# Performance work log

Measured on AMD Instinct MI355X. Metric: run time of the kernel, lower is better.

Reference implementation:

```python
import jax, jax.numpy as jnp
import numpy as np

B, L, S, D, H, TOPK = 8, 2048, 1000, 1024, 8, 10
E = D // H  # d_keys = 128


def setup_inputs() -> dict:
    key = jax.random.key(0)
    ks = jax.random.split(key, 8)
    s = 1.0 / np.sqrt(D)
    return {
        "target_embedding": jax.random.normal(ks[0], (B, L, D), dtype=jnp.float32),
        "source_embedding": jax.random.normal(ks[1], (S, D), dtype=jnp.float32),
        "Wq": jax.random.normal(ks[2], (D, D), dtype=jnp.float32) * s,
        "bq": jnp.zeros((D,), dtype=jnp.float32),
        "Wk": jax.random.normal(ks[3], (D, D), dtype=jnp.float32) * s,
        "bk": jnp.zeros((D,), dtype=jnp.float32),
        "Wo": jax.random.normal(ks[4], (D, D), dtype=jnp.float32) * s,
        "bo": jnp.zeros((D,), dtype=jnp.float32),
        "data_id": 0,
    }


def reference(target_embedding, source_embedding, Wq, bq, Wk, bk, Wo, bo, data_id):
    # data_id is unused by the original module's math.
    b, l, d = target_embedding.shape
    h, e, topk = H, E, TOPK
    scale = 1.0 / np.sqrt(e)

    q = (target_embedding @ Wq + bq).reshape(b, l, h, e)   # [B,L,H,E]
    k = (source_embedding @ Wk + bk).reshape(-1, h, e)      # [S,H,E]

    scores = jnp.einsum('blhe,she->bhls', q, k)             # [B,H,L,S]
    A = jax.nn.softmax(scale * scores, axis=-1)             # dropout is eval-mode identity
    tmps = A.sum(axis=2)                                    # [B,H,S] head-wise column mass
    _, idxs = jax.lax.top_k(tmps, topk)                     # [B,H,topk]

    kh = jnp.transpose(k, (1, 0, 2))                        # [H,S,E]
    # gather per (batch, head) the topk source key vectors
    tok = kh[jnp.arange(h)[None, :, None], idxs, :]         # [B,H,topk,E]
    tok = jnp.transpose(tok, (0, 2, 1, 3)).reshape(b, topk, h * e)  # [B,topk,D]
    return tok @ Wo + bo                                    # [B,topk,D]
```

## Files before the change

kernel.cpp:

```cpp
#include <hip/hip_runtime.h>
#include <hip/hip_bf16.h>
#include <math.h>

constexpr int B_ = 8;
constexpr int L_ = 2048;
constexpr int S_ = 1000;
constexpr int D_ = 1024;
constexpr int H_ = 8;
constexpr int E_ = 128;
constexpr int TOPK_ = 10;
constexpr float SCALE_LOG2E_ = 0.12751744f;

typedef __attribute__((ext_vector_type(8))) short short8;
typedef __attribute__((ext_vector_type(4))) float f32x4;

__device__ inline unsigned short f2bf(float x) {
    unsigned u = __float_as_uint(x);
    unsigned r = (u + 0x7fffu + ((u >> 16) & 1u)) >> 16;
    return (unsigned short)r;
}
__device__ inline float bf2f(unsigned short s) {
    return __uint_as_float(((unsigned)s) << 16);
}

__device__ __forceinline__ float fexp2(float x) {
#if __has_builtin(__builtin_amdgcn_exp2f)
    return __builtin_amdgcn_exp2f(x);
#else
    return __expf(x * 0.69314718056f);
#endif
}

typedef __attribute__((address_space(1))) const unsigned int gas_u32;
typedef __attribute__((address_space(3))) unsigned int las_u32;
__device__ __forceinline__ void gload_lds16(const void* g, void* l) {
    __builtin_amdgcn_global_load_lds((gas_u32*)g, (las_u32*)l, 16, 0, 0);
}

__global__ __launch_bounds__(256) void gemm_bias_kernel(
    const float* __restrict__ A, const float* __restrict__ Bm,
    const float* __restrict__ bias, float* __restrict__ C,
    int M, int N, int Kd)
{
    __shared__ float As[16][65];
    __shared__ float Bs[16][68];

    const int t  = threadIdx.x;
    const int tx = t & 15;
    const int ty = t >> 4;
    const int m0 = blockIdx.y * 64;
    const int n0 = blockIdx.x * 64;

    float acc[4][4];
#pragma unroll
    for (int i = 0; i < 4; ++i)
#pragma unroll
        for (int j = 0; j < 4; ++j) acc[i][j] = 0.f;

    for (int k0 = 0; k0 < Kd; k0 += 16) {
        {
            const int row = t >> 2;
            const int c4  = (t & 3) * 4;
            float4 v = {0.f, 0.f, 0.f, 0.f};
            if (m0 + row < M)
                v = *(const float4*)&A[(size_t)(m0 + row) * Kd + k0 + c4];
            As[c4 + 0][row] = v.x;
            As[c4 + 1][row] = v.y;
            As[c4 + 2][row] = v.z;
            As[c4 + 3][row] = v.w;
        }
        {
            const int row = t >> 4;
            const int c4  = (t & 15) * 4;
            float4 v = *(const float4*)&Bm[(size_t)(k0 + row) * N + n0 + c4];
            *(float4*)&Bs[row][c4] = v;
        }
        __syncthreads();
#pragma unroll
        for (int k = 0; k < 16; ++k) {
            float a[4], b[4];
#pragma unroll
            for (int i = 0; i < 4; ++i) a[i] = As[k][ty * 4 + i];
            float4 bv = *(const float4*)&Bs[k][tx * 4];
            b[0] = bv.x; b[1] = bv.y; b[2] = bv.z; b[3] = bv.w;
#pragma unroll
            for (int i = 0; i < 4; ++i)
#pragma unroll
                for (int j = 0; j < 4; ++j) acc[i][j] += a[i] * b[j];
        }
        __syncthreads();
    }

#pragma unroll
    for (int i = 0; i < 4; ++i) {
        const int row = m0 + ty * 4 + i;
        if (row < M) {
#pragma unroll
            for (int j = 0; j < 4; ++j) {
                const int col = n0 + tx * 4 + j;
                C[(size_t)row * N + col] = acc[i][j] + bias[col];
            }
        }
    }
}

__global__ __launch_bounds__(256) void splitWT_kernel(
    const float* __restrict__ W,
    unsigned short* __restrict__ WTh, unsigned short* __restrict__ WTl)
{
    __shared__ __attribute__((aligned(16))) float tile[64][68];
    const int t  = threadIdx.x;
    const int k0 = blockIdx.y * 64, n0 = blockIdx.x * 64;
#pragma unroll
    for (int it = 0; it < 4; ++it) {
        int id = it * 256 + t;
        int r = id >> 4, c = id & 15;
        *(float4*)&tile[r][c * 4] = *(const float4*)&W[(size_t)(k0 + r) * D_ + n0 + c * 4];
    }
    __syncthreads();
#pragma unroll
    for (int it = 0; it < 4; ++it) {
        int id = it * 256 + t;
        int n = id >> 4, c = id & 15;
        unsigned short hs[4], ls[4];
#pragma unroll
        for (int i = 0; i < 4; ++i) {
            float x = tile[c * 4 + i][n];
            hs[i] = f2bf(x);
            ls[i] = f2bf(x - bf2f(hs[i]));
        }
        size_t o = (size_t)(n0 + n) * D_ + k0 + c * 4;
        uint2 uh; uh.x = (unsigned)hs[0] | ((unsigned)hs[1] << 16);
                  uh.y = (unsigned)hs[2] | ((unsigned)hs[3] << 16);
        uint2 ul; ul.x = (unsigned)ls[0] | ((unsigned)ls[1] << 16);
                  ul.y = (unsigned)ls[2] | ((unsigned)ls[3] << 16);
        *(uint2*)&WTh[o] = uh;
        *(uint2*)&WTl[o] = ul;
    }
}

__global__ __launch_bounds__(256) void split_src_kernel(
    const float* __restrict__ src,
    unsigned short* __restrict__ Sh, unsigned short* __restrict__ Sl)
{
    int idx  = blockIdx.x * 256 + threadIdx.x;
    int base = idx * 4;
    int row  = base >> 10;
    float4 v = {0.f, 0.f, 0.f, 0.f};
    if (row < S_) v = *(const float4*)&src[base];
    float xs[4] = {v.x, v.y, v.z, v.w};
    unsigned short hs[4], ls[4];
#pragma unroll
    for (int i = 0; i < 4; ++i) {
        hs[i] = f2bf(xs[i]);
        ls[i] = f2bf(xs[i] - bf2f(hs[i]));
    }
    uint2 uh; uh.x = (unsigned)hs[0] | ((unsigned)hs[1] << 16);
              uh.y = (unsigned)hs[2] | ((unsigned)hs[3] << 16);
    uint2 ul; ul.x = (unsigned)ls[0] | ((unsigned)ls[1] << 16);
              ul.y = (unsigned)ls[2] | ((unsigned)ls[3] << 16);
    *(uint2*)&Sh[base] = uh;
    *(uint2*)&Sl[base] = ul;
}

__global__ __launch_bounds__(256, 2) void kproj_kernel(
    const unsigned short* __restrict__ Sh, const unsigned short* __restrict__ Sl,
    const unsigned short* __restrict__ WkTh, const unsigned short* __restrict__ WkTl,
    const float* __restrict__ bk,
    float* __restrict__ Kbuf,
    unsigned short* __restrict__ Kh, unsigned short* __restrict__ Kl)
{
    __shared__ __attribute__((aligned(16))) unsigned short Ah[128 * 64];
    __shared__ __attribute__((aligned(16))) unsigned short Al[128 * 64];
    __shared__ __attribute__((aligned(16))) unsigned short Bh[128 * 64];
    __shared__ __attribute__((aligned(16))) unsigned short Bl[128 * 64];

    const int t    = threadIdx.x;
    const int lane = t & 63, w = t >> 6;
    const int mb   = blockIdx.x >> 3;
    const int n0   = (blockIdx.x & 7) * 128;

    f32x4 acc[2][8];
#pragma unroll
    for (int m = 0; m < 2; ++m)
#pragma unroll
        for (int n = 0; n < 8; ++n) acc[m][n] = (f32x4){0.f, 0.f, 0.f, 0.f};

    for (int k0 = 0; k0 < D_; k0 += 64) {
        __syncthreads();
#pragma unroll
        for (int it = 0; it < 4; ++it) {
            int r = it * 32 + (t >> 3), c = t & 7;
            size_t gofs = (size_t)r * D_ + k0 + ((c ^ (r & 7)) << 3);
            int db = it * 4096 + t * 16;
            gload_lds16(&Sh[(size_t)(mb * 128) * D_ + gofs], (char*)Ah + db);
            gload_lds16(&Sl[(size_t)(mb * 128) * D_ + gofs], (char*)Al + db);
            gload_lds16(&WkTh[(size_t)n0 * D_ + gofs], (char*)Bh + db);
            gload_lds16(&WkTl[(size_t)n0 * D_ + gofs], (char*)Bl + db);
        }
        __syncthreads();

#pragma unroll
        for (int ki = 0; ki < 2; ++ki) {
            short8 ah[2], al[2];
#pragma unroll
            for (int m = 0; m < 2; ++m) {
                int r = w * 32 + m * 16 + (lane & 15);
                int slot = ki * 4 + (lane >> 4);
                int lofs = r * 64 + ((slot ^ (r & 7)) << 3);
                ah[m] = *(short8*)&Ah[lofs];
                al[m] = *(short8*)&Al[lofs];
            }
#pragma unroll
            for (int n = 0; n < 8; ++n) {
                int nn = n * 16 + (lane & 15);
                int slot = ki * 4 + (lane >> 4);
                int lofs = nn * 64 + ((slot ^ (nn & 7)) << 3);
                short8 bh = *(short8*)&Bh[lofs];
                short8 bl = *(short8*)&Bl[lofs];
#pragma unroll
                for (int m = 0; m < 2; ++m) {
                    acc[m][n] = __builtin_amdgcn_mfma_f32_16x16x32_bf16(ah[m], bh, acc[m][n], 0, 0, 0);
                    acc[m][n] = __builtin_amdgcn_mfma_f32_16x16x32_bf16(ah[m], bl, acc[m][n], 0, 0, 0);
                    acc[m][n] = __builtin_amdgcn_mfma_f32_16x16x32_bf16(al[m], bh, acc[m][n], 0, 0, 0);
                }
            }
        }
    }

#pragma unroll
    for (int n = 0; n < 8; ++n) {
        int col = n0 + n * 16 + (lane & 15);
        float bkv = bk[col];
#pragma unroll
        for (int m = 0; m < 2; ++m) {
            int rbase = mb * 128 + w * 32 + m * 16 + ((lane >> 4) << 2);
#pragma unroll
            for (int r = 0; r < 4; ++r) {
                int row = rbase + r;
                unsigned short hh = 0, ll = 0;
                if (row < S_) {
                    float kv = acc[m][n][r] + bkv;
                    Kbuf[(size_t)row * D_ + col] = kv;
                    hh = f2bf(kv);
                    ll = f2bf(kv - bf2f(hh));
                }
                Kh[(size_t)row * D_ + col] = hh;
                Kl[(size_t)row * D_ + col] = ll;
            }
        }
    }
}

__global__ __launch_bounds__(256, 2) void qproj_kernel(
    const float* __restrict__ tgt,
    const unsigned short* __restrict__ WqTh, const unsigned short* __restrict__ WqTl,
    const float* __restrict__ bq,
    unsigned short* __restrict__ qhb, unsigned short* __restrict__ qlb)
{
    __shared__ __attribute__((aligned(16))) float          Af[2][128 * 32];
    __shared__ __attribute__((aligned(16))) unsigned short Bh[2][128 * 32];
    __shared__ __attribute__((aligned(16))) unsigned short Bl[2][128 * 32];

    const int t    = threadIdx.x;
    const int lane = t & 63, w = t >> 6;
    const int x    = blockIdx.x & 7;
    const int jj   = blockIdx.x >> 3;
    const int n0   = (jj & 7) * 128;
    const int mb   = (jj >> 3) * 8 + x;

    f32x4 acc[2][8];
#pragma unroll
    for (int m = 0; m < 2; ++m)
#pragma unroll
        for (int n = 0; n < 8; ++n) acc[m][n] = (f32x4){0.f, 0.f, 0.f, 0.f};

#define QP_ISSUE(KT, BUF)                                                   \
    do {                                                                    \
        _Pragma("unroll")                                                   \
        for (int it = 0; it < 4; ++it) {                       \
            int id = it * 256 + t;                                          \
            int line = id >> 4, sub = id & 15;                              \
            int gs = sub ^ (line & 15);                                     \
            size_t ga = (size_t)(mb * 128 + line * 2 + (gs >> 3)) * D_      \
                        + (KT) * 32 + ((gs & 7) << 2);                      \
            gload_lds16(&tgt[ga], (char*)&Af[(BUF)][0] + id * 16);          \
        }                                                                   \
        _Pragma("unroll")                                                   \
        for (int it = 0; it < 2; ++it) {                      \
            int id = it * 256 + t;                                          \
            int line = id >> 4, sub = id & 15;                              \
            int gs = sub ^ (line & 15);                                     \
            size_t gb = (size_t)(n0 + line * 4 + (gs >> 2)) * D_            \
                        + (KT) * 32 + ((gs & 3) << 3);                      \
            gload_lds16(&WqTh[gb], (char*)&Bh[(BUF)][0] + id * 16);         \
            gload_lds16(&WqTl[gb], (char*)&Bl[(BUF)][0] + id * 16);         \
        }                                                                   \
    } while (0)

    QP_ISSUE(0, 0);
    int cur = 0;
    for (int kt = 0; kt < 32; ++kt) {
        __syncthreads();
        if (kt < 31) QP_ISSUE(kt + 1, cur ^ 1);

        short8 ah[2], al[2];
#pragma unroll
        for (int m = 0; m < 2; ++m) {
            int r    = w * 32 + m * 16 + (lane & 15);
            int c0   = (lane >> 4) * 2;
            int line = r >> 1;
            int sub0 = (r & 1) * 8 + c0;
            float4 x0 = *(float4*)&Af[cur][line * 64 + ((sub0 ^ (line & 15)) << 2)];
            float4 x1 = *(float4*)&Af[cur][line * 64 + (((sub0 + 1) ^ (line & 15)) << 2)];
            float xs[8] = {x0.x, x0.y, x0.z, x0.w, x1.x, x1.y, x1.z, x1.w};
#pragma unroll
            for (int jjj = 0; jjj < 8; ++jjj) {
                unsigned short hh = f2bf(xs[jjj]);
                ah[m][jjj] = (short)hh;
                al[m][jjj] = (short)f2bf(xs[jjj] - bf2f(hh));
            }
        }
#pragma unroll
        for (int n = 0; n < 8; ++n) {
            int nn   = n * 16 + (lane & 15);
            int line = nn >> 2;
            int sub  = (nn & 3) * 4 + (lane >> 4);
            int lofs = line * 128 + ((sub ^ (line & 15)) << 3);
            short8 bh = *(short8*)&Bh[cur][lofs];
            short8 bl = *(short8*)&Bl[cur][lofs];
#pragma unroll
            for (int m = 0; m < 2; ++m) {
                acc[m][n] = __builtin_amdgcn_mfma_f32_16x16x32_bf16(ah[m], bh, acc[m][n], 0, 0, 0);
                acc[m][n] = __builtin_amdgcn_mfma_f32_16x16x32_bf16(ah[m], bl, acc[m][n], 0, 0, 0);
                acc[m][n] = __builtin_amdgcn_mfma_f32_16x16x32_bf16(al[m], bh, acc[m][n], 0, 0, 0);
            }
        }
        cur ^= 1;
    }
#undef QP_ISSUE

#pragma unroll
    for (int n = 0; n < 8; ++n) {
        int col = n0 + n * 16 + (lane & 15);
        float bqv = bq[col];
#pragma unroll
        for (int m = 0; m < 2; ++m) {
            int rbase = mb * 128 + w * 32 + m * 16 + ((lane >> 4) << 2);
#pragma unroll
            for (int r = 0; r < 4; ++r) {
                float q = (acc[m][n][r] + bqv) * SCALE_LOG2E_;
                unsigned short hh = f2bf(q);
                qhb[(size_t)(rbase + r) * D_ + col] = hh;
                qlb[(size_t)(rbase + r) * D_ + col] = f2bf(q - bf2f(hh));
            }
        }
    }
}

__global__ __launch_bounds__(256, 2) void scores2p_kernel(
    const unsigned short* __restrict__ qhb, const unsigned short* __restrict__ qlb,
    const unsigned short* __restrict__ Kh, const unsigned short* __restrict__ Kl,
    float* __restrict__ tmps, int b0)
{
    __shared__ __attribute__((aligned(16))) unsigned short SH[2][32 * 128];
    __shared__ __attribute__((aligned(16))) unsigned short SL[2][32 * 128];
    __shared__ float tmps_l[1024];

    const int t    = threadIdx.x;
    const int lane = t & 63, w = t >> 6;
    const int blk  = blockIdx.x;
    const int bb   = blk >> 6;
    const int h    = (blk >> 3) & 7;
    const int lt   = blk & 7;
    const int qrow0 = bb * L_ + lt * 256;
    const int bh_i  = (b0 + bb) * H_ + h;
    const int kr0   = t >> 4;
    const int kc0   = t & 15;

    for (int i = t; i < 1024; i += 256) tmps_l[i] = 0.f;

#define SC_ISSUE0(ST, BUF)                                                  \
    do {                                                                    \
        _Pragma("unroll")                                                   \
        for (int it = 0; it < 4; ++it) {                                    \
            int r = it * 16 + kr0;                                          \
            size_t g = (size_t)((ST) * 64 + r) * D_ + h * E_                \
                       + ((kc0 ^ (r & 15)) << 3);                           \
            char* base = (it < 2) ? (char*)&SH[(BUF)][0]                    \
                                  : (char*)&SL[(BUF)][0];                   \
            int db = (it & 1) * 4096 + t * 16;                              \
            gload_lds16(&Kh[g], base + db);                                 \
        }                                                                   \
    } while (0)

#define SC_ISSUE2(ST, BUF)                                                  \
    do {                                                                    \
        _Pragma("unroll")                                                   \
        for (int it = 0; it < 2; ++it) {                                    \
            int r = it * 16 + kr0;                                          \
            size_t g = (size_t)((ST) * 32 + r) * D_ + h * E_                \
                       + ((kc0 ^ (r & 15)) << 3);                           \
            int db = it * 4096 + t * 16;                                    \
            gload_lds16(&Kh[g], (char*)&SH[(BUF)][0] + db);                 \
            gload_lds16(&Kl[g], (char*)&SL[(BUF)][0] + db);                 \
        }                                                                   \
    } while (0)

    SC_ISSUE0(0, 1);

    short8 qh[4][4], ql[4][4];
#pragma unroll
    for (int ch = 0; ch < 8; ++ch) {
        __syncthreads();
#pragma unroll
        for (int it = 0; it < 2; ++it) {
            int r = it * 16 + kr0;
            size_t g = (size_t)(qrow0 + ch * 32 + r) * D_ + h * E_ + kc0 * 8;
            int lofs = r * 128 + ((kc0 ^ (r & 15)) << 3);
            *(uint4*)&SH[0][lofs] = *(const uint4*)&qhb[g];
            *(uint4*)&SL[0][lofs] = *(const uint4*)&qlb[g];
        }
        __syncthreads();
        if ((ch >> 1) == w) {
#pragma unroll
            for (int j = 0; j < 2; ++j) {
                int rg = (ch & 1) * 2 + j;
#pragma unroll
                for (int ki = 0; ki < 4; ++ki) {
                    int rq = j * 16 + (lane & 15);
                    int slot = ki * 4 + (lane >> 4);
                    int lofs = rq * 128 + ((slot ^ (rq & 15)) << 3);
                    qh[rg][ki] = *(short8*)&SH[0][lofs];
                    ql[rg][ki] = *(short8*)&SL[0][lofs];
                }
            }
        }
    }

    float zacc[4][4];
#pragma unroll
    for (int rg = 0; rg < 4; ++rg)
#pragma unroll
        for (int r = 0; r < 4; ++r) zacc[rg][r] = 0.f;
    float invZ[4][4];

    int cur = 1;

    for (int u = 0; u < 16; ++u) {
        __syncthreads();
        if (u < 15) SC_ISSUE0(u + 1, cur ^ 1);
        else        SC_ISSUE2(0, cur ^ 1);

#pragma unroll
        for (int nfh = 0; nfh < 2; ++nfh) {
            f32x4 acc[4][2];
#pragma unroll
            for (int rg = 0; rg < 4; ++rg)
#pragma unroll
                for (int n2 = 0; n2 < 2; ++n2) acc[rg][n2] = (f32x4){0.f, 0.f, 0.f, 0.f};

#pragma unroll
            for (int ki = 0; ki < 4; ++ki)
#pragma unroll
                for (int n2 = 0; n2 < 2; ++n2) {
                    int nf = nfh * 2 + n2;
                    int sr = nf * 16 + (lane & 15);
                    int slot = ki * 4 + (lane >> 4);
                    int lofs = (sr & 31) * 128 + ((slot ^ (sr & 15)) << 3);
                    short8 bh = (nf < 2) ? *(short8*)&SH[cur][lofs]
                                         : *(short8*)&SL[cur][lofs];
#pragma unroll
                    for (int rg = 0; rg < 4; ++rg)
                        acc[rg][n2] = __builtin_amdgcn_mfma_f32_16x16x32_bf16(qh[rg][ki], bh, acc[rg][n2], 0, 0, 0);
                }

#pragma unroll
            for (int n2 = 0; n2 < 2; ++n2) {
                int s = u * 64 + (nfh * 2 + n2) * 16 + (lane & 15);
                if (s < S_) {
#pragma unroll
                    for (int rg = 0; rg < 4; ++rg)
#pragma unroll
                        for (int r = 0; r < 4; ++r)
                            zacc[rg][r] += fexp2(acc[rg][n2][r]);
                }
            }
        }

        if (u == 15) {
#pragma unroll
            for (int rg = 0; rg < 4; ++rg)
#pragma unroll
                for (int r = 0; r < 4; ++r) {
                    float z = zacc[rg][r];
                    z += __shfl_xor(z, 1);
                    z += __shfl_xor(z, 2);
                    z += __shfl_xor(z, 4);
                    z += __shfl_xor(z, 8);
                    invZ[rg][r] = 1.f / z;
                }
        }
        cur ^= 1;
    }

    for (int u = 0; u < 32; ++u) {
        __syncthreads();
        if (u < 31) SC_ISSUE2(u + 1, cur ^ 1);

        f32x4 acc[4][2];
#pragma unroll
        for (int rg = 0; rg < 4; ++rg)
#pragma unroll
            for (int nf = 0; nf < 2; ++nf) acc[rg][nf] = (f32x4){0.f, 0.f, 0.f, 0.f};

#pragma unroll
        for (int ki = 0; ki < 4; ++ki)
#pragma unroll
            for (int nf = 0; nf < 2; ++nf) {
                int sr = nf * 16 + (lane & 15);
                int slot = ki * 4 + (lane >> 4);
                int lofs = sr * 128 + ((slot ^ (sr & 15)) << 3);
                short8 bh = *(short8*)&SH[cur][lofs];
                short8 bl = *(short8*)&SL[cur][lofs];
#pragma unroll
                for (int rg = 0; rg < 4; ++rg) {
                    acc[rg][nf] = __builtin_amdgcn_mfma_f32_16x16x32_bf16(qh[rg][ki], bh, acc[rg][nf], 0, 0, 0);
                    acc[rg][nf] = __builtin_amdgcn_mfma_f32_16x16x32_bf16(qh[rg][ki], bl, acc[rg][nf], 0, 0, 0);
                    acc[rg][nf] = __builtin_amdgcn_mfma_f32_16x16x32_bf16(ql[rg][ki], bh, acc[rg][nf], 0, 0, 0);
                }
            }

#pragma unroll
        for (int nf = 0; nf < 2; ++nf) {
            int s = u * 32 + nf * 16 + (lane & 15);
            if (s < S_) {
                float val = 0.f;
#pragma unroll
                for (int rg = 0; rg < 4; ++rg)
#pragma unroll
                    for (int r = 0; r < 4; ++r)
                        val += fexp2(acc[rg][nf][r]) * invZ[rg][r];
                atomicAdd(&tmps_l[s], val);
            }
        }
        cur ^= 1;
    }
#undef SC_ISSUE0
#undef SC_ISSUE2

    __syncthreads();
    for (int i = t; i < S_; i += 256)
        atomicAdd(&tmps[(size_t)bh_i * S_ + i], tmps_l[i]);
}

__global__ __launch_bounds__(256) void topk_kernel(
    const float* __restrict__ tmps, int* __restrict__ idxs)
{
    const int bh = blockIdx.x;
    const int t  = threadIdx.x;
    __shared__ float v[S_];
    __shared__ float rv[256];
    __shared__ int   ri[256];

    for (int i = t; i < S_; i += 256) v[i] = tmps[(size_t)bh * S_ + i];
    __syncthreads();

    for (int it = 0; it < TOPK_; ++it) {
        float best = -1e38f;
        int bi = 0x7fffffff;
        for (int s = t; s < S_; s += 256) {
            const float x = v[s];
            if (x > best) { best = x; bi = s; }
        }
        rv[t] = best; ri[t] = bi;
        __syncthreads();
        for (int k = 128; k > 0; k >>= 1) {
            if (t < k) {
                const float x = rv[t + k];
                const int  xi = ri[t + k];
                if (x > rv[t] || (x == rv[t] && xi < ri[t])) { rv[t] = x; ri[t] = xi; }
            }
            __syncthreads();
        }
        if (t == 0) {
            idxs[bh * TOPK_ + it] = ri[0];
            v[ri[0]] = -1e38f;
        }
        __syncthreads();
    }
}

__global__ __launch_bounds__(256) void gather_kernel(
    const float* __restrict__ K, const int* __restrict__ idxs,
    float* __restrict__ tok)
{
    const int o = blockIdx.x * 256 + threadIdx.x;
    if (o >= B_ * TOPK_ * D_) return;
    const int d  = o & (D_ - 1);
    const int tt = (o >> 10) % TOPK_;
    const int b  = o / (D_ * TOPK_);
    const int h  = d >> 7;
    const int s  = idxs[(b * H_ + h) * TOPK_ + tt];
    tok[o] = K[(size_t)s * D_ + d];
}

extern "C" void kernel_launch(void* const* d_in, const int* in_sizes, int n_in,
                              void* d_out, int out_size, void* d_ws, size_t ws_size,
                              hipStream_t stream)
{
    const float* tgt = (const float*)d_in[0];
    const float* src = (const float*)d_in[1];
    const float* Wq  = (const float*)d_in[2];
    const float* bq  = (const float*)d_in[3];
    const float* Wk  = (const float*)d_in[4];
    const float* bk  = (const float*)d_in[5];
    const float* Wo  = (const float*)d_in[6];
    const float* bo  = (const float*)d_in[7];
    float* out = (float*)d_out;

    char* ws = (char*)d_ws;
    size_t off = 0;
    float*          Kbuf = (float*)(ws + off);          off += (size_t)S_ * D_ * 4;
    float*          tmps = (float*)(ws + off);          off += (size_t)B_ * H_ * S_ * 4;
    int*            idxs = (int*)(ws + off);            off += (size_t)B_ * H_ * TOPK_ * 4;
    off = (off + 255) & ~(size_t)255;
    float*          tok  = (float*)(ws + off);          off += (size_t)B_ * TOPK_ * D_ * 4;
    unsigned short* Kh   = (unsigned short*)(ws + off); off += (size_t)1024 * D_ * 2;
    unsigned short* Kl   = (unsigned short*)(ws + off); off += (size_t)1024 * D_ * 2;
    unsigned short* WqTh = (unsigned short*)(ws + off); off += (size_t)D_ * D_ * 2;
    unsigned short* WqTl = (unsigned short*)(ws + off); off += (size_t)D_ * D_ * 2;
    unsigned short* WkTh = (unsigned short*)(ws + off); off += (size_t)D_ * D_ * 2;
    unsigned short* WkTl = (unsigned short*)(ws + off); off += (size_t)D_ * D_ * 2;
    unsigned short* Sh   = (unsigned short*)(ws + off); off += (size_t)1024 * D_ * 2;
    unsigned short* Sl   = (unsigned short*)(ws + off); off += (size_t)1024 * D_ * 2;
    unsigned short* planes = (unsigned short*)(ws + off);
    const size_t fixed_bytes = off;
    const size_t plane_elems_per_b = (size_t)L_ * D_;

    int nb_fit = 1;
    if (ws_size > fixed_bytes) {
        size_t f = (ws_size - fixed_bytes) / (2 * plane_elems_per_b * 2);
        nb_fit = (f < 1) ? 1 : (f > 8 ? 8 : (int)f);
    }

    hipMemsetAsync(tmps, 0, (size_t)B_ * H_ * S_ * sizeof(float), stream);

    split_src_kernel<<<(1024 * D_) / (256 * 4), 256, 0, stream>>>(src, Sh, Sl);
    {
        dim3 g(D_ / 64, D_ / 64);
        splitWT_kernel<<<g, 256, 0, stream>>>(Wq, WqTh, WqTl);
        splitWT_kernel<<<g, 256, 0, stream>>>(Wk, WkTh, WkTl);
    }

    kproj_kernel<<<64, 256, 0, stream>>>(Sh, Sl, WkTh, WkTl, bk, Kbuf, Kh, Kl);

    for (int b0 = 0; b0 < B_; b0 += nb_fit) {
        int nb = (B_ - b0 < nb_fit) ? (B_ - b0) : nb_fit;
        unsigned short* qhb = planes;
        unsigned short* qlb = qhb + (size_t)nb_fit * plane_elems_per_b;

        qproj_kernel<<<nb * 128, 256, 0, stream>>>(
            tgt + (size_t)b0 * L_ * D_, WqTh, WqTl, bq, qhb, qlb);
        scores2p_kernel<<<nb * 64, 256, 0, stream>>>(qhb, qlb, Kh, Kl, tmps, b0);
    }

    topk_kernel<<<B_ * H_, 256, 0, stream>>>(tmps, idxs);
    gather_kernel<<<(B_ * TOPK_ * D_ + 255) / 256, 256, 0, stream>>>(Kbuf, idxs, tok);
    {
        dim3 g(D_ / 64, (B_ * TOPK_ + 63) / 64);
        gemm_bias_kernel<<<g, 256, 0, stream>>>(tok, Wo, bo, out, B_ * TOPK_, D_, D_);
    }
}
```

Before: 381.9 us.

## Load Q-projection activations to registers and enlarge score-pass K tiles

The Q projection no longer stages fp32 activations through shared memory. It loads them straight from global memory into registers, double-buffered across an explicitly unrolled pair of k-steps, and raises the occupancy hint to 3 blocks per CU because LDS use drops. The scores kernel's second pass now processes 64 source rows per stage in a unified 4-plane LDS buffer instead of 32, halving the barrier and issue count. The trade-off is higher register pressure and uncoalesced per-lane global reads of the activations.

```diff
diff --git a/kernel.cpp b/kernel.cpp
--- a/kernel.cpp
+++ b/kernel.cpp
@@ -252,13 +252,12 @@
     }
 }
 
-__global__ __launch_bounds__(256, 2) void qproj_kernel(
+__global__ __launch_bounds__(256, 3) void qproj_kernel(
     const float* __restrict__ tgt,
     const unsigned short* __restrict__ WqTh, const unsigned short* __restrict__ WqTl,
     const float* __restrict__ bq,
     unsigned short* __restrict__ qhb, unsigned short* __restrict__ qlb)
 {
-    __shared__ __attribute__((aligned(16))) float          Af[2][128 * 32];
     __shared__ __attribute__((aligned(16))) unsigned short Bh[2][128 * 32];
     __shared__ __attribute__((aligned(16))) unsigned short Bl[2][128 * 32];
 
@@ -275,19 +274,10 @@
 #pragma unroll
         for (int n = 0; n < 8; ++n) acc[m][n] = (f32x4){0.f, 0.f, 0.f, 0.f};
 
-#define QP_ISSUE(KT, BUF)                                                   \
+#define QB_ISSUE(KT, BUF)                                                   \
     do {                                                                    \
         _Pragma("unroll")                                                   \
-        for (int it = 0; it < 4; ++it) {                       \
-            int id = it * 256 + t;                                          \
-            int line = id >> 4, sub = id & 15;                              \
-            int gs = sub ^ (line & 15);                                     \
-            size_t ga = (size_t)(mb * 128 + line * 2 + (gs >> 3)) * D_      \
-                        + (KT) * 32 + ((gs & 7) << 2);                      \
-            gload_lds16(&tgt[ga], (char*)&Af[(BUF)][0] + id * 16);          \
-        }                                                                   \
-        _Pragma("unroll")                                                   \
-        for (int it = 0; it < 2; ++it) {                      \
+        for (int it = 0; it < 2; ++it) {                                    \
             int id = it * 256 + t;                                          \
             int line = id >> 4, sub = id & 15;                              \
             int gs = sub ^ (line & 15);                                     \
@@ -298,47 +288,65 @@
         }                                                                   \
     } while (0)
 
-    QP_ISSUE(0, 0);
-    int cur = 0;
-    for (int kt = 0; kt < 32; ++kt) {
-        __syncthreads();
-        if (kt < 31) QP_ISSUE(kt + 1, cur ^ 1);
-
-        short8 ah[2], al[2];
-#pragma unroll
-        for (int m = 0; m < 2; ++m) {
-            int r    = w * 32 + m * 16 + (lane & 15);
-            int c0   = (lane >> 4) * 2;
-            int line = r >> 1;
-            int sub0 = (r & 1) * 8 + c0;
-            float4 x0 = *(float4*)&Af[cur][line * 64 + ((sub0 ^ (line & 15)) << 2)];
-            float4 x1 = *(float4*)&Af[cur][line * 64 + (((sub0 + 1) ^ (line & 15)) << 2)];
-            float xs[8] = {x0.x, x0.y, x0.z, x0.w, x1.x, x1.y, x1.z, x1.w};
-#pragma unroll
-            for (int jjj = 0; jjj < 8; ++jjj) {
-                unsigned short hh = f2bf(xs[jjj]);
-                ah[m][jjj] = (short)hh;
-                al[m][jjj] = (short)f2bf(xs[jjj] - bf2f(hh));
-            }
-        }
-#pragma unroll
-        for (int n = 0; n < 8; ++n) {
-            int nn   = n * 16 + (lane & 15);
-            int line = nn >> 2;
-            int sub  = (nn & 3) * 4 + (lane >> 4);
-            int lofs = line * 128 + ((sub ^ (line & 15)) << 3);
-            short8 bh = *(short8*)&Bh[cur][lofs];
-            short8 bl = *(short8*)&Bl[cur][lofs];
-#pragma unroll
-            for (int m = 0; m < 2; ++m) {
-                acc[m][n] = __builtin_amdgcn_mfma_f32_16x16x32_bf16(ah[m], bh, acc[m][n], 0, 0, 0);
-                acc[m][n] = __builtin_amdgcn_mfma_f32_16x16x32_bf16(ah[m], bl, acc[m][n], 0, 0, 0);
-                acc[m][n] = __builtin_amdgcn_mfma_f32_16x16x32_bf16(al[m], bh, acc[m][n], 0, 0, 0);
-            }
-        }
-        cur ^= 1;
-    }
-#undef QP_ISSUE
+#define QA_LOAD(KT, XA)                                                     \
+    do {                                                                    \
+        _Pragma("unroll")                                                   \
+        for (int m = 0; m < 2; ++m) {                                       \
+            int r = mb * 128 + w * 32 + m * 16 + (lane & 15);               \
+            const float* ga = &tgt[(size_t)r * D_ + (KT) * 32 + (lane >> 4) * 8]; \
+            XA[m][0] = *(const float4*)ga;                                  \
+            XA[m][1] = *(const float4*)(ga + 4);                            \
+        }                                                                   \
+    } while (0)
+
+#define QP_COMPUTE(XA, BUF)                                                 \
+    do {                                                                    \
+        short8 ah[2], al[2];                                                \
+        _Pragma("unroll")                                                   \
+        for (int m = 0; m < 2; ++m) {                                       \
+            float xs[8] = {XA[m][0].x, XA[m][0].y, XA[m][0].z, XA[m][0].w,  \
+                           XA[m][1].x, XA[m][1].y, XA[m][1].z, XA[m][1].w}; \
+            _Pragma("unroll")                                               \
+            for (int j = 0; j < 8; ++j) {                                   \
+                unsigned short hh = f2bf(xs[j]);                            \
+                ah[m][j] = (short)hh;                                       \
+                al[m][j] = (short)f2bf(xs[j] - bf2f(hh));                   \
+            }                                                               \
+        }                                                                   \
+        _Pragma("unroll")                                                   \
+        for (int n = 0; n < 8; ++n) {                                       \
+            int nn   = n * 16 + (lane & 15);                                \
+            int line = nn >> 2;                                             \
+            int sub  = (nn & 3) * 4 + (lane >> 4);                          \
+            int lofs = line * 128 + ((sub ^ (line & 15)) << 3);             \
+            short8 bh = *(short8*)&Bh[(BUF)][lofs];                         \
+            short8 bl = *(short8*)&Bl[(BUF)][lofs];                         \
+            _Pragma("unroll")                                               \
+            for (int m = 0; m < 2; ++m) {                                   \
+                acc[m][n] = __builtin_amdgcn_mfma_f32_16x16x32_bf16(ah[m], bh, acc[m][n], 0, 0, 0); \
+                acc[m][n] = __builtin_amdgcn_mfma_f32_16x16x32_bf16(ah[m], bl, acc[m][n], 0, 0, 0); \
+                acc[m][n] = __builtin_amdgcn_mfma_f32_16x16x32_bf16(al[m], bh, acc[m][n], 0, 0, 0); \
+            }                                                               \
+        }                                                                   \
+    } while (0)
+
+    float4 xa0[2][2], xa1[2][2];
+    QB_ISSUE(0, 0);
+    QA_LOAD(0, xa0);
+
+#pragma unroll 1
+    for (int kt2 = 0; kt2 < 16; ++kt2) {
+        const int kt = kt2 * 2;
+        __syncthreads();
+        if (kt + 1 < 32) { QB_ISSUE(kt + 1, 1); QA_LOAD(kt + 1, xa1); }
+        QP_COMPUTE(xa0, 0);
+        __syncthreads();
+        if (kt + 2 < 32) { QB_ISSUE(kt + 2, 0); QA_LOAD(kt + 2, xa0); }
+        QP_COMPUTE(xa1, 1);
+    }
+#undef QB_ISSUE
+#undef QA_LOAD
+#undef QP_COMPUTE
 
 #pragma unroll
     for (int n = 0; n < 8; ++n) {
@@ -363,8 +371,7 @@
     const unsigned short* __restrict__ Kh, const unsigned short* __restrict__ Kl,
     float* __restrict__ tmps, int b0)
 {
-    __shared__ __attribute__((aligned(16))) unsigned short SH[2][32 * 128];
-    __shared__ __attribute__((aligned(16))) unsigned short SL[2][32 * 128];
+    __shared__ __attribute__((aligned(16))) unsigned short KB[2][4][32 * 128];
     __shared__ float tmps_l[1024];
 
     const int t    = threadIdx.x;
@@ -387,23 +394,22 @@
             int r = it * 16 + kr0;                                          \
             size_t g = (size_t)((ST) * 64 + r) * D_ + h * E_                \
                        + ((kc0 ^ (r & 15)) << 3);                           \
-            char* base = (it < 2) ? (char*)&SH[(BUF)][0]                    \
-                                  : (char*)&SL[(BUF)][0];                   \
             int db = (it & 1) * 4096 + t * 16;                              \
-            gload_lds16(&Kh[g], base + db);                                 \
+            gload_lds16(&Kh[g], (char*)&KB[(BUF)][it >> 1][0] + db);        \
         }                                                                   \
     } while (0)
 
-#define SC_ISSUE2(ST, BUF)                                                  \
+#define SC_ISSUE1(ST, BUF)                                                  \
     do {                                                                    \
         _Pragma("unroll")                                                   \
-        for (int it = 0; it < 2; ++it) {                                    \
+        for (int it = 0; it < 4; ++it) {                                    \
             int r = it * 16 + kr0;                                          \
-            size_t g = (size_t)((ST) * 32 + r) * D_ + h * E_                \
+            size_t g = (size_t)((ST) * 64 + r) * D_ + h * E_                \
                        + ((kc0 ^ (r & 15)) << 3);                           \
-            int db = it * 4096 + t * 16;                                    \
-            gload_lds16(&Kh[g], (char*)&SH[(BUF)][0] + db);                 \
-            gload_lds16(&Kl[g], (char*)&SL[(BUF)][0] + db);                 \
+            int pl = it >> 1;                                               \
+            int db = (it & 1) * 4096 + t * 16;                              \
+            gload_lds16(&Kh[g], (char*)&KB[(BUF)][pl][0] + db);             \
+            gload_lds16(&Kl[g], (char*)&KB[(BUF)][pl + 2][0] + db);         \
         }                                                                   \
     } while (0)
 
@@ -418,8 +424,8 @@
             int r = it * 16 + kr0;
             size_t g = (size_t)(qrow0 + ch * 32 + r) * D_ + h * E_ + kc0 * 8;
             int lofs = r * 128 + ((kc0 ^ (r & 15)) << 3);
-            *(uint4*)&SH[0][lofs] = *(const uint4*)&qhb[g];
-            *(uint4*)&SL[0][lofs] = *(const uint4*)&qlb[g];
+            *(uint4*)&KB[0][0][lofs] = *(const uint4*)&qhb[g];
+            *(uint4*)&KB[0][1][lofs] = *(const uint4*)&qlb[g];
         }
         __syncthreads();
         if ((ch >> 1) == w) {
@@ -431,8 +437,8 @@
                     int rq = j * 16 + (lane & 15);
                     int slot = ki * 4 + (lane >> 4);
                     int lofs = rq * 128 + ((slot ^ (rq & 15)) << 3);
-                    qh[rg][ki] = *(short8*)&SH[0][lofs];
-                    ql[rg][ki] = *(short8*)&SL[0][lofs];
+                    qh[rg][ki] = *(short8*)&KB[0][0][lofs];
+                    ql[rg][ki] = *(short8*)&KB[0][1][lofs];
                 }
             }
         }
@@ -450,7 +456,7 @@
     for (int u = 0; u < 16; ++u) {
         __syncthreads();
         if (u < 15) SC_ISSUE0(u + 1, cur ^ 1);
-        else        SC_ISSUE2(0, cur ^ 1);
+        else        SC_ISSUE1(0, cur ^ 1);
 
 #pragma unroll
         for (int nfh = 0; nfh < 2; ++nfh) {
@@ -468,8 +474,7 @@
                     int sr = nf * 16 + (lane & 15);
                     int slot = ki * 4 + (lane >> 4);
                     int lofs = (sr & 31) * 128 + ((slot ^ (sr & 15)) << 3);
-                    short8 bh = (nf < 2) ? *(short8*)&SH[cur][lofs]
-                                         : *(short8*)&SL[cur][lofs];
+                    short8 bh = *(short8*)&KB[cur][sr >> 5][lofs];
 #pragma unroll
                     for (int rg = 0; rg < 4; ++rg)
                         acc[rg][n2] = __builtin_amdgcn_mfma_f32_16x16x32_bf16(qh[rg][ki], bh, acc[rg][n2], 0, 0, 0);
@@ -504,50 +509,55 @@
         cur ^= 1;
     }
 
-    for (int u = 0; u < 32; ++u) {
-        __syncthreads();
-        if (u < 31) SC_ISSUE2(u + 1, cur ^ 1);
-
-        f32x4 acc[4][2];
-#pragma unroll
-        for (int rg = 0; rg < 4; ++rg)
-#pragma unroll
-            for (int nf = 0; nf < 2; ++nf) acc[rg][nf] = (f32x4){0.f, 0.f, 0.f, 0.f};
-
-#pragma unroll
-        for (int ki = 0; ki < 4; ++ki)
-#pragma unroll
-            for (int nf = 0; nf < 2; ++nf) {
-                int sr = nf * 16 + (lane & 15);
-                int slot = ki * 4 + (lane >> 4);
-                int lofs = sr * 128 + ((slot ^ (sr & 15)) << 3);
-                short8 bh = *(short8*)&SH[cur][lofs];
-                short8 bl = *(short8*)&SL[cur][lofs];
-#pragma unroll
-                for (int rg = 0; rg < 4; ++rg) {
-                    acc[rg][nf] = __builtin_amdgcn_mfma_f32_16x16x32_bf16(qh[rg][ki], bh, acc[rg][nf], 0, 0, 0);
-                    acc[rg][nf] = __builtin_amdgcn_mfma_f32_16x16x32_bf16(qh[rg][ki], bl, acc[rg][nf], 0, 0, 0);
-                    acc[rg][nf] = __builtin_amdgcn_mfma_f32_16x16x32_bf16(ql[rg][ki], bh, acc[rg][nf], 0, 0, 0);
-                }
-            }
-
-#pragma unroll
-        for (int nf = 0; nf < 2; ++nf) {
-            int s = u * 32 + nf * 16 + (lane & 15);
-            if (s < S_) {
-                float val = 0.f;
-#pragma unroll
-                for (int rg = 0; rg < 4; ++rg)
-#pragma unroll
-                    for (int r = 0; r < 4; ++r)
-                        val += fexp2(acc[rg][nf][r]) * invZ[rg][r];
-                atomicAdd(&tmps_l[s], val);
+    for (int u = 0; u < 16; ++u) {
+        __syncthreads();
+        if (u < 15) SC_ISSUE1(u + 1, cur ^ 1);
+
+#pragma unroll
+        for (int nfh = 0; nfh < 2; ++nfh) {
+            f32x4 acc[4][2];
+#pragma unroll
+            for (int rg = 0; rg < 4; ++rg)
+#pragma unroll
+                for (int n2 = 0; n2 < 2; ++n2) acc[rg][n2] = (f32x4){0.f, 0.f, 0.f, 0.f};
+
+#pragma unroll
+            for (int ki = 0; ki < 4; ++ki)
+#pragma unroll
+                for (int n2 = 0; n2 < 2; ++n2) {
+                    int nf = nfh * 2 + n2;
+                    int sr = nf * 16 + (lane & 15);
+                    int pl = sr >> 5;
+                    int slot = ki * 4 + (lane >> 4);
+                    int lofs = (sr & 31) * 128 + ((slot ^ (sr & 15)) << 3);
+                    short8 bh = *(short8*)&KB[cur][pl][lofs];
+                    short8 bl = *(short8*)&KB[cur][pl + 2][lofs];
+#pragma unroll
+                    for (int rg = 0; rg < 4; ++rg) {
+                        acc[rg][n2] = __builtin_amdgcn_mfma_f32_16x16x32_bf16(qh[rg][ki], bh, acc[rg][n2], 0, 0, 0);
+                        acc[rg][n2] = __builtin_amdgcn_mfma_f32_16x16x32_bf16(qh[rg][ki], bl, acc[rg][n2], 0, 0, 0);
+                        acc[rg][n2] = __builtin_amdgcn_mfma_f32_16x16x32_bf16(ql[rg][ki], bh, acc[rg][n2], 0, 0, 0);
+                    }
+                }
+
+#pragma unroll
+            for (int n2 = 0; n2 < 2; ++n2) {
+                int s = u * 64 + (nfh * 2 + n2) * 16 + (lane & 15);
+                if (s < S_) {
+                    float val = 0.f;
+#pragma unroll
+                    for (int rg = 0; rg < 4; ++rg)
+#pragma unroll
+                        for (int r = 0; r < 4; ++r)
+                            val += fexp2(acc[rg][n2][r]) * invZ[rg][r];
+                    atomicAdd(&tmps_l[s], val);
+                }
             }
         }
         cur ^= 1;
     }
 #undef SC_ISSUE0
-#undef SC_ISSUE2
+#undef SC_ISSUE1
 
     __syncthreads();
     for (int i = t; i < S_; i += 256)
```

After: 385.9 us. About the same (+1.0%).
